# Optimization experiments

Hardware: AMD Instinct MI355X
Metric: run time of the kernel (lower is better)

Reference implementation:

```python
import jax, jax.numpy as jnp
import numpy as np

B, N, IN_DIM, HEADS, PER_HEAD = 8, 512, 256, 4, 32
OUT_DIM = HEADS * PER_HEAD  # 128
NEG_SLOPE = 0.2


def setup_inputs() -> dict:
    key = jax.random.key(0)
    ks = jax.random.split(key, 8)
    x = jax.random.normal(ks[0], (B, N, IN_DIM), jnp.float32)
    adj = jax.random.randint(ks[1], (B, N, N), 0, 2, jnp.int32)
    sl = 1.0 / np.sqrt(IN_DIM)
    W_l = jax.random.normal(ks[2], (IN_DIM, OUT_DIM), jnp.float32) * sl  # source proj
    b_l = jnp.zeros((OUT_DIM,), jnp.float32)
    W_r = jax.random.normal(ks[3], (IN_DIM, OUT_DIM), jnp.float32) * sl  # target proj
    b_r = jnp.zeros((OUT_DIM,), jnp.float32)
    att = jax.random.normal(ks[4], (HEADS, PER_HEAD), jnp.float32) * (1.0 / np.sqrt(PER_HEAD))
    bias = jnp.zeros((OUT_DIM,), jnp.float32)
    return {"x": x, "adj": adj, "W_l": W_l, "b_l": b_l, "W_r": W_r, "b_r": b_r,
            "att": att, "bias": bias}


def _gatv2_single(x_b, adj_b, W_l, b_l, W_r, b_r, att, bias):
    # PyG GATv2Conv: remove_self_loops + add_self_loops -> diagonal forced to 1
    n = x_b.shape[0]
    adj_sl = jnp.fill_diagonal(adj_b, 1, inplace=False)
    # edge_index = adj.nonzero().t(): source = row, target = col
    m = (adj_sl != 0).T  # m[i, j]: source j feeds target i
    xl = (x_b @ W_l + b_l).reshape(n, HEADS, PER_HEAD)  # source-side features
    xr = (x_b @ W_r + b_r).reshape(n, HEADS, PER_HEAD)  # target-side features
    s = xr[:, None] + xl[None, :]                       # [i, j, H, C]
    s = jnp.where(s > 0, s, NEG_SLOPE * s)              # LeakyReLU(0.2)
    e = jnp.einsum('ijhc,hc->ijh', s, att)              # attention logits
    e = jnp.where(m[..., None], e, -jnp.inf)
    alpha = jax.nn.softmax(e, axis=1)                   # softmax over sources j
    out = jnp.einsum('ijh,jhc->ihc', alpha, xl).reshape(n, HEADS * PER_HEAD)
    return out + bias


def reference(x, adj, W_l, b_l, W_r, b_r, att, bias):
    # Sequential per-batch processing, faithful to the original Python loop
    # and keeping the [N,N,H,C] intermediate to one graph at a time.
    def one(args):
        x_b, adj_b = args
        return _gatv2_single(x_b, adj_b, W_l, b_l, W_r, b_r, att, bias)
    return jax.lax.map(one, (x, adj))  # [B, N, OUT_DIM]
```

## Files before the change

kernel.cpp:

```cpp
#include <hip/hip_runtime.h>

#define B_   8
#define N_   512
#define IND  256
#define H_   4
#define PH   32
#define OD   128
#define TI   4

typedef float v2f __attribute__((ext_vector_type(2)));

#define ATT_SCALE 0.5770780163555854f
#define DLR_SCALE 0.8656170245333781f

template <int PAT>
__device__ __forceinline__ float dpp_add(float x) {
    int yi = __builtin_amdgcn_mov_dpp(__float_as_int(x), PAT, 0xF, 0xF, true);
    return x + __int_as_float(yi);
}

__device__ __forceinline__ float fast_exp2(float x) {
#if __has_builtin(__builtin_amdgcn_exp2f)
    return __builtin_amdgcn_exp2f(x);
#else
    return exp2f(x);
#endif
}

__device__ __forceinline__ void pk_fma(v2f& d, v2f a, v2f b) {
    asm("v_pk_fma_f32 %0, %1, %2, %0" : "+v"(d) : "v"(a), "v"(b));
}

template <int HI>
__device__ __forceinline__ void pk_fma_bc(v2f& d, v2f a, v2f b) {
    if constexpr (HI == 0)
        asm("v_pk_fma_f32 %0, %1, %2, %0 op_sel:[0,0,0] op_sel_hi:[0,1,1]"
            : "+v"(d) : "v"(a), "v"(b));
    else
        asm("v_pk_fma_f32 %0, %1, %2, %0 op_sel:[1,0,0] op_sel_hi:[1,1,1]"
            : "+v"(d) : "v"(a), "v"(b));
}

__device__ __forceinline__ v2f pk_add(v2f a, v2f b) {
    v2f d;
    asm("v_pk_add_f32 %0, %1, %2" : "=v"(d) : "v"(a), "v"(b));
    return d;
}

__global__ __launch_bounds__(512, 2) void proj_kernel(
    const float* __restrict__ x,
    const float* __restrict__ Wl, const float* __restrict__ bl,
    const float* __restrict__ Wr, const float* __restrict__ br,
    const float* __restrict__ att,
    float* __restrict__ xl, float* __restrict__ xr,
    float* __restrict__ dl, float* __restrict__ dr)
{
    __shared__ float xs[8 * IND];
    __shared__ float comb[8][64][33];

    const int t = threadIdx.x;
    const int row0 = blockIdx.x * 8;

    ((float4*)xs)[t] = ((const float4*)(x + (size_t)row0 * IND))[t];
    __syncthreads();

    const int og    = t & 31;
    const int ks    = (t >> 5) & 7;
    const int which = t >> 8;
    const int o0 = og * 4;
    const int k0 = ks * 32;
    const float* W = (which ? Wr : Wl) + (size_t)k0 * OD + o0;

    #pragma unroll 1
    for (int rep = 0; rep < 2; ++rep) {
        asm volatile("" ::: "memory");
        __syncthreads();

        v2f acc2[8][2];
        #pragma unroll
        for (int r = 0; r < 8; ++r) {
            acc2[r][0] = (v2f){0.f, 0.f};
            acc2[r][1] = (v2f){0.f, 0.f};
        }

        float4 wb[2][2];
        wb[0][0] = *(const float4*)(W);
        wb[0][1] = *(const float4*)(W + OD);

        #pragma unroll 2
        for (int s = 0; s < 16; ++s) {
            const int cur = s & 1, nxt = cur ^ 1;
            if (s < 15) {
                const float* Wq = W + (size_t)(2 * (s + 1)) * OD;
                wb[nxt][0] = *(const float4*)(Wq);
                wb[nxt][1] = *(const float4*)(Wq + OD);
            }
            v2f w0lo = (v2f){wb[cur][0].x, wb[cur][0].y};
            v2f w0hi = (v2f){wb[cur][0].z, wb[cur][0].w};
            v2f w1lo = (v2f){wb[cur][1].x, wb[cur][1].y};
            v2f w1hi = (v2f){wb[cur][1].z, wb[cur][1].w};
            #pragma unroll
            for (int r = 0; r < 8; ++r) {
                float2 xv = *(const float2*)(&xs[r * IND + k0 + 2 * s]);
                v2f xp = (v2f){xv.x, xv.y};
                pk_fma_bc<0>(acc2[r][0], xp, w0lo);
                pk_fma_bc<0>(acc2[r][1], xp, w0hi);
                pk_fma_bc<1>(acc2[r][0], xp, w1lo);
                pk_fma_bc<1>(acc2[r][1], xp, w1hi);
            }
        }

        const int pid = og | (which << 5);
        #pragma unroll
        for (int r = 0; r < 8; ++r) {
            comb[ks][pid][r * 4 + 0] = acc2[r][0].x;
            comb[ks][pid][r * 4 + 1] = acc2[r][0].y;
            comb[ks][pid][r * 4 + 2] = acc2[r][1].x;
            comb[ks][pid][r * 4 + 3] = acc2[r][1].y;
        }
        __syncthreads();

        const int ogf = t & 31;
        const int rf  = (t >> 5) & 7;
        const int whf = t >> 8;
        const int pidf = ogf | (whf << 5);
        const float* bb = whf ? br : bl;
        float* dst = whf ? xr : xl;
        float* dp  = whf ? dr : dl;
        float4 bv = *(const float4*)(bb + ogf * 4);
        float4 av = *(const float4*)(att + ogf * 4);
        const float bvf[4] = {bv.x, bv.y, bv.z, bv.w};
        const float avf[4] = {av.x, av.y, av.z, av.w};
        float y[4];
        #pragma unroll
        for (int c = 0; c < 4; ++c) {
            const int idx = rf * 4 + c;
            float s01 = comb[0][pidf][idx] + comb[1][pidf][idx];
            float s23 = comb[2][pidf][idx] + comb[3][pidf][idx];
            float s45 = comb[4][pidf][idx] + comb[5][pidf][idx];
            float s67 = comb[6][pidf][idx] + comb[7][pidf][idx];
            y[c] = ((s01 + s23) + (s45 + s67)) + bvf[c];
        }
        *(float4*)(&dst[(size_t)(row0 + rf) * OD + ogf * 4]) =
            make_float4(y[0], y[1], y[2], y[3]);
        float dc = fmaf(avf[0], y[0], fmaf(avf[1], y[1],
                   fmaf(avf[2], y[2], avf[3] * y[3])));
        dc += __shfl_xor(dc, 1);
        dc += __shfl_xor(dc, 2);
        dc += __shfl_xor(dc, 4);
        if ((ogf & 7) == 0)
            dp[(size_t)(row0 + rf) * H_ + (ogf >> 3)] = DLR_SCALE * dc;
    }
}

__global__ __launch_bounds__(512, 4) void attn_kernel(
    const int* __restrict__ adj, const float* __restrict__ att,
    const float* __restrict__ bias,
    const float* __restrict__ xl, const float* __restrict__ xr,
    const float* __restrict__ dl, const float* __restrict__ dr,
    float* __restrict__ out)
{
    __shared__ float sacc[H_][2][32][PH + 1];
    __shared__ float ssum[H_][32][TI];

    const int t = threadIdx.x;
    const int bid = (blockIdx.x & 7) * 128 + (blockIdx.x >> 3);
    const int b  = bid >> 7;
    const int i0 = (bid & 127) * TI;
    const int cq = t & 3;
    const int js = (t >> 2) & 31;
    const int h  = t >> 7;
    const int cbase = h * PH + cq * 8;

    float atS[8];
    {
        const float* ap = att + cbase;
        float4 a0 = *(const float4*)(ap);
        float4 a1 = *(const float4*)(ap + 4);
        atS[0] = ATT_SCALE * a0.x; atS[1] = ATT_SCALE * a0.y;
        atS[2] = ATT_SCALE * a0.z; atS[3] = ATT_SCALE * a0.w;
        atS[4] = ATT_SCALE * a1.x; atS[5] = ATT_SCALE * a1.y;
        atS[6] = ATT_SCALE * a1.z; atS[7] = ATT_SCALE * a1.w;
    }
    v2f xrv[TI][4];
    #pragma unroll
    for (int il = 0; il < TI; ++il) {
        const float* xp = xr + ((size_t)(b * N_ + i0 + il)) * OD + cbase;
        float4 r0 = *(const float4*)(xp);
        float4 r1 = *(const float4*)(xp + 4);
        xrv[il][0] = (v2f){r0.x, r0.y};
        xrv[il][1] = (v2f){r0.z, r0.w};
        xrv[il][2] = (v2f){r1.x, r1.y};
        xrv[il][3] = (v2f){r1.z, r1.w};
    }

    v2f acc[TI][4];
    float sumw[TI];
    #pragma unroll
    for (int il = 0; il < TI; ++il) {
        sumw[il] = 0.f;
        #pragma unroll
        for (int m = 0; m < 4; ++m) acc[il][m] = (v2f){0.f, 0.f};
    }

    const float* xlp = xl + ((size_t)(b * N_ + js)) * OD + cbase;
    const int*   ajp = adj + ((size_t)(b * N_ + js)) * N_ + i0;
    const float* dlp = dl + ((size_t)(b * N_ + js)) * H_ + h;

    float4 va = *(const float4*)(xlp);
    float4 vb = *(const float4*)(xlp + 4);
    int4   mj = *(const int4*)(ajp);
    float  dj = *dlp;

    #pragma unroll 2
    for (int u = 0; u < 16; ++u) {
        float4 wa = va, wb = vb;
        int4   wm = mj;
        float  wd = dj;
        if (u < 15) {
            xlp += 32 * OD; ajp += 32 * N_; dlp += 32 * H_;
            va = *(const float4*)(xlp);
            vb = *(const float4*)(xlp + 4);
            mj = *(const int4*)(ajp);
            dj = *dlp;
        }
        const int j = u * 32 + js;
        v2f p0 = (v2f){wa.x, wa.y}, p1 = (v2f){wa.z, wa.w};
        v2f p2 = (v2f){wb.x, wb.y}, p3 = (v2f){wb.z, wb.w};
        int wmv[TI] = {wm.x, wm.y, wm.z, wm.w};
        #pragma unroll
        for (int il = 0; il < TI; ++il) {
            v2f s01 = pk_add(xrv[il][0], p0);
            v2f s23 = pk_add(xrv[il][1], p1);
            v2f s45 = pk_add(xrv[il][2], p2);
            v2f s67 = pk_add(xrv[il][3], p3);
            float e2a = 0.f, e2b = 0.f;
            e2a = fmaf(atS[0], __builtin_fabsf(s01.x), e2a);
            e2b = fmaf(atS[1], __builtin_fabsf(s01.y), e2b);
            e2a = fmaf(atS[2], __builtin_fabsf(s23.x), e2a);
            e2b = fmaf(atS[3], __builtin_fabsf(s23.y), e2b);
            e2a = fmaf(atS[4], __builtin_fabsf(s45.x), e2a);
            e2b = fmaf(atS[5], __builtin_fabsf(s45.y), e2b);
            e2a = fmaf(atS[6], __builtin_fabsf(s67.x), e2a);
            e2b = fmaf(atS[7], __builtin_fabsf(s67.y), e2b);
            float eh = e2a + e2b;
            eh = dpp_add<0xB1>(eh);
            eh = dpp_add<0x4E>(eh);
            float e = wd + eh;
            bool keep = (wmv[il] != 0) || (j == i0 + il);
            float w = keep ? fast_exp2(e) : 0.f;
            sumw[il] += w;
            v2f ws = (v2f){w, w};
            pk_fma(acc[il][0], ws, p0);
            pk_fma(acc[il][1], ws, p1);
            pk_fma(acc[il][2], ws, p2);
            pk_fma(acc[il][3], ws, p3);
        }
    }

    if (cq == 0) {
        #pragma unroll
        for (int il = 0; il < TI; ++il)
            ssum[h][js][il] = sumw[il];
    }
    #pragma unroll
    for (int p = 0; p < 2; ++p) {
        *(float4*)(&sacc[h][p][js][cq * 8]) =
            make_float4(acc[p][0].x, acc[p][0].y, acc[p][1].x, acc[p][1].y);
        *(float4*)(&sacc[h][p][js][cq * 8 + 4]) =
            make_float4(acc[p][2].x, acc[p][2].y, acc[p][3].x, acc[p][3].y);
    }
    __syncthreads();
    if (t < 256) {
        const int c   = t & 31;
        const int ilr = (t >> 5) & 1;
        const int hr  = t >> 6;
        float a = 0.f, st = 0.f;
        #pragma unroll
        for (int k = 0; k < 32; ++k) {
            a  += sacc[hr][ilr][k][c];
            st += ssum[hr][k][ilr];
        }
        const int cg = hr * PH + c;
        out[((size_t)(b * N_ + i0 + ilr)) * OD + cg] =
            fmaf(a, 1.f / st, bias[cg]);
    }
    __syncthreads();
    #pragma unroll
    for (int p = 0; p < 2; ++p) {
        *(float4*)(&sacc[h][p][js][cq * 8]) =
            make_float4(acc[2 + p][0].x, acc[2 + p][0].y,
                        acc[2 + p][1].x, acc[2 + p][1].y);
        *(float4*)(&sacc[h][p][js][cq * 8 + 4]) =
            make_float4(acc[2 + p][2].x, acc[2 + p][2].y,
                        acc[2 + p][3].x, acc[2 + p][3].y);
    }
    __syncthreads();
    if (t < 256) {
        const int c   = t & 31;
        const int ilr = (t >> 5) & 1;
        const int hr  = t >> 6;
        float a = 0.f, st = 0.f;
        #pragma unroll
        for (int k = 0; k < 32; ++k) {
            a  += sacc[hr][ilr][k][c];
            st += ssum[hr][k][2 + ilr];
        }
        const int cg = hr * PH + c;
        out[((size_t)(b * N_ + i0 + 2 + ilr)) * OD + cg] =
            fmaf(a, 1.f / st, bias[cg]);
    }
}

extern "C" void kernel_launch(void* const* d_in, const int* in_sizes, int n_in,
                              void* d_out, int out_size, void* d_ws, size_t ws_size,
                              hipStream_t stream) {
    const float* x    = (const float*)d_in[0];
    const int*   adj  = (const int*)d_in[1];
    const float* Wl   = (const float*)d_in[2];
    const float* bl   = (const float*)d_in[3];
    const float* Wr   = (const float*)d_in[4];
    const float* br   = (const float*)d_in[5];
    const float* att  = (const float*)d_in[6];
    const float* bias = (const float*)d_in[7];
    float* out = (float*)d_out;

    float* xl = (float*)d_ws;
    float* xr = xl + (size_t)B_ * N_ * OD;
    float* dl = xr + (size_t)B_ * N_ * OD;
    float* dr = dl + (size_t)B_ * N_ * H_;

    proj_kernel<<<512, 512, 0, stream>>>(x, Wl, bl, Wr, br, att, xl, xr, dl, dr);
    attn_kernel<<<1024, 512, 0, stream>>>(adj, att, bias, xl, xr, dl, dr, out);
}
```

Baseline: 125.6 us.

## Stage attention source tiles in LDS and drop duplicated projection pass

The projection kernel previously ran its whole GEMM-and-store body twice in a redundant loop. That loop is removed, and the weight prefetch is deepened from a two-slot to a four-slot register ring. The attention kernel now cooperatively loads each 32-row chunk of xl, the adjacency ints and dl into a double-buffered LDS tile, instead of having every thread fetch its own slice from global memory. The goal is to cut redundant compute and improve load coalescing, at the cost of one block-wide barrier per iteration and more LDS per block.

```diff
diff --git a/kernel.cpp b/kernel.cpp
--- a/kernel.cpp
+++ b/kernel.cpp
@@ -71,86 +71,83 @@
     const int k0 = ks * 32;
     const float* W = (which ? Wr : Wl) + (size_t)k0 * OD + o0;
 
-    #pragma unroll 1
-    for (int rep = 0; rep < 2; ++rep) {
-        asm volatile("" ::: "memory");
-        __syncthreads();
-
-        v2f acc2[8][2];
+    v2f acc2[8][2];
+    #pragma unroll
+    for (int r = 0; r < 8; ++r) {
+        acc2[r][0] = (v2f){0.f, 0.f};
+        acc2[r][1] = (v2f){0.f, 0.f};
+    }
+
+    float4 wb[4][2];
+    #pragma unroll
+    for (int i = 0; i < 3; ++i) {
+        wb[i][0] = *(const float4*)(W + (size_t)(2 * i) * OD);
+        wb[i][1] = *(const float4*)(W + (size_t)(2 * i + 1) * OD);
+    }
+
+    #pragma unroll 4
+    for (int s = 0; s < 16; ++s) {
+        if (s + 3 < 16) {
+            const float* Wq = W + (size_t)(2 * (s + 3)) * OD;
+            wb[(s + 3) & 3][0] = *(const float4*)(Wq);
+            wb[(s + 3) & 3][1] = *(const float4*)(Wq + OD);
+        }
+        const int cur = s & 3;
+        v2f w0lo = (v2f){wb[cur][0].x, wb[cur][0].y};
+        v2f w0hi = (v2f){wb[cur][0].z, wb[cur][0].w};
+        v2f w1lo = (v2f){wb[cur][1].x, wb[cur][1].y};
+        v2f w1hi = (v2f){wb[cur][1].z, wb[cur][1].w};
         #pragma unroll
         for (int r = 0; r < 8; ++r) {
-            acc2[r][0] = (v2f){0.f, 0.f};
-            acc2[r][1] = (v2f){0.f, 0.f};
-        }
-
-        float4 wb[2][2];
-        wb[0][0] = *(const float4*)(W);
-        wb[0][1] = *(const float4*)(W + OD);
-
-        #pragma unroll 2
-        for (int s = 0; s < 16; ++s) {
-            const int cur = s & 1, nxt = cur ^ 1;
-            if (s < 15) {
-                const float* Wq = W + (size_t)(2 * (s + 1)) * OD;
-                wb[nxt][0] = *(const float4*)(Wq);
-                wb[nxt][1] = *(const float4*)(Wq + OD);
-            }
-            v2f w0lo = (v2f){wb[cur][0].x, wb[cur][0].y};
-            v2f w0hi = (v2f){wb[cur][0].z, wb[cur][0].w};
-            v2f w1lo = (v2f){wb[cur][1].x, wb[cur][1].y};
-            v2f w1hi = (v2f){wb[cur][1].z, wb[cur][1].w};
-            #pragma unroll
-            for (int r = 0; r < 8; ++r) {
-                float2 xv = *(const float2*)(&xs[r * IND + k0 + 2 * s]);
-                v2f xp = (v2f){xv.x, xv.y};
-                pk_fma_bc<0>(acc2[r][0], xp, w0lo);
-                pk_fma_bc<0>(acc2[r][1], xp, w0hi);
-                pk_fma_bc<1>(acc2[r][0], xp, w1lo);
-                pk_fma_bc<1>(acc2[r][1], xp, w1hi);
-            }
-        }
-
-        const int pid = og | (which << 5);
-        #pragma unroll
-        for (int r = 0; r < 8; ++r) {
-            comb[ks][pid][r * 4 + 0] = acc2[r][0].x;
-            comb[ks][pid][r * 4 + 1] = acc2[r][0].y;
-            comb[ks][pid][r * 4 + 2] = acc2[r][1].x;
-            comb[ks][pid][r * 4 + 3] = acc2[r][1].y;
-        }
-        __syncthreads();
-
-        const int ogf = t & 31;
-        const int rf  = (t >> 5) & 7;
-        const int whf = t >> 8;
-        const int pidf = ogf | (whf << 5);
-        const float* bb = whf ? br : bl;
-        float* dst = whf ? xr : xl;
-        float* dp  = whf ? dr : dl;
-        float4 bv = *(const float4*)(bb + ogf * 4);
-        float4 av = *(const float4*)(att + ogf * 4);
-        const float bvf[4] = {bv.x, bv.y, bv.z, bv.w};
-        const float avf[4] = {av.x, av.y, av.z, av.w};
-        float y[4];
-        #pragma unroll
-        for (int c = 0; c < 4; ++c) {
-            const int idx = rf * 4 + c;
-            float s01 = comb[0][pidf][idx] + comb[1][pidf][idx];
-            float s23 = comb[2][pidf][idx] + comb[3][pidf][idx];
-            float s45 = comb[4][pidf][idx] + comb[5][pidf][idx];
-            float s67 = comb[6][pidf][idx] + comb[7][pidf][idx];
-            y[c] = ((s01 + s23) + (s45 + s67)) + bvf[c];
-        }
-        *(float4*)(&dst[(size_t)(row0 + rf) * OD + ogf * 4]) =
-            make_float4(y[0], y[1], y[2], y[3]);
-        float dc = fmaf(avf[0], y[0], fmaf(avf[1], y[1],
-                   fmaf(avf[2], y[2], avf[3] * y[3])));
-        dc += __shfl_xor(dc, 1);
-        dc += __shfl_xor(dc, 2);
-        dc += __shfl_xor(dc, 4);
-        if ((ogf & 7) == 0)
-            dp[(size_t)(row0 + rf) * H_ + (ogf >> 3)] = DLR_SCALE * dc;
-    }
+            float2 xv = *(const float2*)(&xs[r * IND + k0 + 2 * s]);
+            v2f xp = (v2f){xv.x, xv.y};
+            pk_fma_bc<0>(acc2[r][0], xp, w0lo);
+            pk_fma_bc<0>(acc2[r][1], xp, w0hi);
+            pk_fma_bc<1>(acc2[r][0], xp, w1lo);
+            pk_fma_bc<1>(acc2[r][1], xp, w1hi);
+        }
+    }
+
+    const int pid = og | (which << 5);
+    #pragma unroll
+    for (int r = 0; r < 8; ++r) {
+        comb[ks][pid][r * 4 + 0] = acc2[r][0].x;
+        comb[ks][pid][r * 4 + 1] = acc2[r][0].y;
+        comb[ks][pid][r * 4 + 2] = acc2[r][1].x;
+        comb[ks][pid][r * 4 + 3] = acc2[r][1].y;
+    }
+    __syncthreads();
+
+    const int ogf = t & 31;
+    const int rf  = (t >> 5) & 7;
+    const int whf = t >> 8;
+    const int pidf = ogf | (whf << 5);
+    const float* bb = whf ? br : bl;
+    float* dst = whf ? xr : xl;
+    float* dp  = whf ? dr : dl;
+    float4 bv = *(const float4*)(bb + ogf * 4);
+    float4 av = *(const float4*)(att + ogf * 4);
+    const float bvf[4] = {bv.x, bv.y, bv.z, bv.w};
+    const float avf[4] = {av.x, av.y, av.z, av.w};
+    float y[4];
+    #pragma unroll
+    for (int c = 0; c < 4; ++c) {
+        const int idx = rf * 4 + c;
+        float s01 = comb[0][pidf][idx] + comb[1][pidf][idx];
+        float s23 = comb[2][pidf][idx] + comb[3][pidf][idx];
+        float s45 = comb[4][pidf][idx] + comb[5][pidf][idx];
+        float s67 = comb[6][pidf][idx] + comb[7][pidf][idx];
+        y[c] = ((s01 + s23) + (s45 + s67)) + bvf[c];
+    }
+    *(float4*)(&dst[(size_t)(row0 + rf) * OD + ogf * 4]) =
+        make_float4(y[0], y[1], y[2], y[3]);
+    float dc = fmaf(avf[0], y[0], fmaf(avf[1], y[1],
+               fmaf(avf[2], y[2], avf[3] * y[3])));
+    dc += __shfl_xor(dc, 1);
+    dc += __shfl_xor(dc, 2);
+    dc += __shfl_xor(dc, 4);
+    if ((ogf & 7) == 0)
+        dp[(size_t)(row0 + rf) * H_ + (ogf >> 3)] = DLR_SCALE * dc;
 }
 
 __global__ __launch_bounds__(512, 4) void attn_kernel(
@@ -160,8 +157,10 @@
     const float* __restrict__ dl, const float* __restrict__ dr,
     float* __restrict__ out)
 {
-    __shared__ float sacc[H_][2][32][PH + 1];
-    __shared__ float ssum[H_][32][TI];
+    __shared__ __attribute__((aligned(16))) char lds_raw[36864];
+    float (*xls)[32][129] = (float (*)[32][129])(lds_raw);
+    int4  (*adjs)[32]     = (int4  (*)[32])(lds_raw + 33024);
+    float (*dls)[32][4]   = (float (*)[32][4])(lds_raw + 34048);
 
     const int t = threadIdx.x;
     const int bid = (blockIdx.x & 7) * 128 + (blockIdx.x >> 3);
@@ -203,30 +202,52 @@
         for (int m = 0; m < 4; ++m) acc[il][m] = (v2f){0.f, 0.f};
     }
 
-    const float* xlp = xl + ((size_t)(b * N_ + js)) * OD + cbase;
-    const int*   ajp = adj + ((size_t)(b * N_ + js)) * N_ + i0;
-    const float* dlp = dl + ((size_t)(b * N_ + js)) * H_ + h;
-
-    float4 va = *(const float4*)(xlp);
-    float4 vb = *(const float4*)(xlp + 4);
-    int4   mj = *(const int4*)(ajp);
-    float  dj = *dlp;
+    const int fr0 = t >> 5;
+    const int fs  = (t & 31) * 4;
+    const float* xlbase = xl + (size_t)(b * N_) * OD;
+    const int*   ajbase = adj + (size_t)(b * N_) * N_ + i0;
+    const float* dlbase = dl + (size_t)(b * N_) * H_;
+
+    {
+        float4 x0 = *(const float4*)(xlbase + (size_t)fr0 * OD + fs);
+        float4 x1 = *(const float4*)(xlbase + (size_t)(fr0 + 16) * OD + fs);
+        int4 a = {0, 0, 0, 0}; float4 d = {0.f, 0.f, 0.f, 0.f};
+        if (t < 32) {
+            a = *(const int4*)(ajbase + (size_t)t * N_);
+            d = *(const float4*)(dlbase + t * H_);
+        }
+        float* w0 = &xls[0][fr0][fs];
+        w0[0] = x0.x; w0[1] = x0.y; w0[2] = x0.z; w0[3] = x0.w;
+        float* w1 = &xls[0][fr0 + 16][fs];
+        w1[0] = x1.x; w1[1] = x1.y; w1[2] = x1.z; w1[3] = x1.w;
+        if (t < 32) { adjs[0][t] = a; *(float4*)dls[0][t] = d; }
+    }
+    __syncthreads();
 
     #pragma unroll 2
     for (int u = 0; u < 16; ++u) {
-        float4 wa = va, wb = vb;
-        int4   wm = mj;
-        float  wd = dj;
-        if (u < 15) {
-            xlp += 32 * OD; ajp += 32 * N_; dlp += 32 * H_;
-            va = *(const float4*)(xlp);
-            vb = *(const float4*)(xlp + 4);
-            mj = *(const int4*)(ajp);
-            dj = *dlp;
-        }
+        const int cur = u & 1, nxt = cur ^ 1;
+
+        float4 x0 = {0.f, 0.f, 0.f, 0.f}, x1 = {0.f, 0.f, 0.f, 0.f};
+        int4 a = {0, 0, 0, 0}; float4 d = {0.f, 0.f, 0.f, 0.f};
+        if (u + 1 < 16) {
+            const float* sb = xlbase + (size_t)((u + 1) * 32) * OD;
+            x0 = *(const float4*)(sb + (size_t)fr0 * OD + fs);
+            x1 = *(const float4*)(sb + (size_t)(fr0 + 16) * OD + fs);
+            if (t < 32) {
+                a = *(const int4*)(ajbase + (size_t)((u + 1) * 32 + t) * N_);
+                d = *(const float4*)(dlbase + ((u + 1) * 32 + t) * H_);
+            }
+        }
+
+        float p[8];
+        #pragma unroll
+        for (int e = 0; e < 8; ++e) p[e] = xls[cur][js][cbase + e];
+        int4  wm = adjs[cur][js];
+        float wd = dls[cur][js][h];
         const int j = u * 32 + js;
-        v2f p0 = (v2f){wa.x, wa.y}, p1 = (v2f){wa.z, wa.w};
-        v2f p2 = (v2f){wb.x, wb.y}, p3 = (v2f){wb.z, wb.w};
+        v2f p0 = (v2f){p[0], p[1]}, p1 = (v2f){p[2], p[3]};
+        v2f p2 = (v2f){p[4], p[5]}, p3 = (v2f){p[6], p[7]};
         int wmv[TI] = {wm.x, wm.y, wm.z, wm.w};
         #pragma unroll
         for (int il = 0; il < TI; ++il) {
@@ -256,7 +277,19 @@
             pk_fma(acc[il][2], ws, p2);
             pk_fma(acc[il][3], ws, p3);
         }
-    }
+
+        if (u + 1 < 16) {
+            float* w0 = &xls[nxt][fr0][fs];
+            w0[0] = x0.x; w0[1] = x0.y; w0[2] = x0.z; w0[3] = x0.w;
+            float* w1 = &xls[nxt][fr0 + 16][fs];
+            w1[0] = x1.x; w1[1] = x1.y; w1[2] = x1.z; w1[3] = x1.w;
+            if (t < 32) { adjs[nxt][t] = a; *(float4*)dls[nxt][t] = d; }
+        }
+        __syncthreads();
+    }
+
+    float (*sacc)[2][32][PH + 1] = (float (*)[2][32][PH + 1])(lds_raw);
+    float (*ssum)[32][TI]        = (float (*)[32][TI])(lds_raw + 33792);
 
     if (cq == 0) {
         #pragma unroll
@@ -275,15 +308,15 @@
         const int c   = t & 31;
         const int ilr = (t >> 5) & 1;
         const int hr  = t >> 6;
-        float a = 0.f, st = 0.f;
+        float av = 0.f, st = 0.f;
         #pragma unroll
         for (int k = 0; k < 32; ++k) {
-            a  += sacc[hr][ilr][k][c];
+            av += sacc[hr][ilr][k][c];
             st += ssum[hr][k][ilr];
         }
         const int cg = hr * PH + c;
         out[((size_t)(b * N_ + i0 + ilr)) * OD + cg] =
-            fmaf(a, 1.f / st, bias[cg]);
+            fmaf(av, 1.f / st, bias[cg]);
     }
     __syncthreads();
     #pragma unroll
@@ -300,15 +333,15 @@
         const int c   = t & 31;
         const int ilr = (t >> 5) & 1;
         const int hr  = t >> 6;
-        float a = 0.f, st = 0.f;
+        float av = 0.f, st = 0.f;
         #pragma unroll
         for (int k = 0; k < 32; ++k) {
-            a  += sacc[hr][ilr][k][c];
+            av += sacc[hr][ilr][k][c];
             st += ssum[hr][k][2 + ilr];
         }
         const int cg = hr * PH + c;
         out[((size_t)(b * N_ + i0 + 2 + ilr)) * OD + cg] =
-            fmaf(a, 1.f / st, bias[cg]);
+            fmaf(av, 1.f / st, bias[cg]);
     }
 }
 
```

New measurement: 151.0 us. +20.2%, slower.
